# Performance work log

Hardware: AMD Instinct MI355X
Metric: run time of the kernel (lower is better)

The kernel has to match this reference:

```python
import jax, jax.numpy as jnp
import numpy as np

N_NODES = 500_000
N_EDGES = 1_000_000
EMB = 64           # config.Model.embedding_size
F = 128            # config.Model.latency_feature_size
L = 8              # config.Latency.latency_feature_length
OP_CNT = 5000
SV_CNT = 2000
ST_CNT = 16
IN_DIM = 3 * EMB + L  # 200


def setup_inputs() -> dict:
    key = jax.random.key(0)
    ks = jax.random.split(key, 24)
    s = 0.02
    inp = {
        'operation_id': jax.random.randint(ks[0], (N_NODES,), 0, OP_CNT, dtype=jnp.int32),
        'service_id':   jax.random.randint(ks[1], (N_NODES,), 0, SV_CNT, dtype=jnp.int32),
        'status_id':    jax.random.randint(ks[2], (N_NODES,), 0, ST_CNT, dtype=jnp.int32),
        'latency_feat': jax.random.normal(ks[3], (N_NODES, L), dtype=jnp.float32),
        'edge_src':     jax.random.randint(ks[4], (N_EDGES,), 0, N_NODES, dtype=jnp.int32),
        'edge_dst':     jax.random.randint(ks[5], (N_EDGES,), 0, N_NODES, dtype=jnp.int32),
        'eps':          jax.random.normal(ks[6], (N_NODES, F), dtype=jnp.float32),
        # parameters (LevelEmbedding + TreeLSTMLatencyEncoder + TreeLSTMLatencyDecoder)
        'op_embed':      jax.random.normal(ks[7],  (OP_CNT, EMB), dtype=jnp.float32) * s,
        'service_embed': jax.random.normal(ks[8],  (SV_CNT, EMB), dtype=jnp.float32) * s,
        'status_embed':  jax.random.normal(ks[9],  (ST_CNT, EMB), dtype=jnp.float32) * s,
        'enc_W1': jax.random.normal(ks[10], (IN_DIM, F), dtype=jnp.float32) * s,
        'enc_b1': jnp.zeros((F,), dtype=jnp.float32),
        'enc_W2': jax.random.normal(ks[11], (F, 2 * F), dtype=jnp.float32) * s,
        'enc_b2': jnp.zeros((2 * F,), dtype=jnp.float32),
        'dec_Wself': jax.random.normal(ks[12], (F, F), dtype=jnp.float32) * s,
        'dec_Wagg':  jax.random.normal(ks[13], (F, F), dtype=jnp.float32) * s,
        'mu_W': jax.random.normal(ks[14], (F, L), dtype=jnp.float32) * s,
        'mu_b': jnp.zeros((L,), dtype=jnp.float32),
        'lv_W': jax.random.normal(ks[15], (F, L), dtype=jnp.float32) * s,
        'lv_b': jnp.zeros((L,), dtype=jnp.float32),
        'opwise_embed': jax.random.normal(ks[16], (OP_CNT + 1, 2 * L * L), dtype=jnp.float32) * s,
    }
    return inp


def reference(operation_id, service_id, status_id, latency_feat, edge_src, edge_dst, eps,
              op_embed, service_embed, status_embed,
              enc_W1, enc_b1, enc_W2, enc_b2,
              dec_Wself, dec_Wagg, mu_W, mu_b, lv_W, lv_b, opwise_embed):
    N = latency_feat.shape[0]
    # ---- LevelEmbedding: gathers + concat ----
    feats = jnp.concatenate([
        op_embed[operation_id],
        service_embed[service_id],
        status_embed[status_id],
        latency_feat,
    ], axis=-1)  # [N, 3*EMB + L]
    # ---- TreeLSTMLatencyEncoder ----
    h = jax.nn.relu(feats @ enc_W1 + enc_b1)
    y = h @ enc_W2 + enc_b2                       # [N, 2F]
    z_mu, z_lv = jnp.split(y, 2, axis=-1)
    z_lv = jnp.tanh(z_lv)
    z = z_mu + jnp.exp(0.5 * z_lv) * eps          # reparameterize, [N, F]
    # ---- TreeLSTM decoder (one child-sum message-passing step over edges) ----
    agg = jax.ops.segment_sum(z[edge_src], edge_dst, num_segments=N)  # scatter-reduce
    yd = jax.nn.relu(z @ dec_Wself + agg @ dec_Wagg)                  # [N, F]
    mu = yd @ mu_W + mu_b   # [N, L]
    lv = yd @ lv_W + lv_b   # [N, L]
    # op-wise output transform: per-node [1,L] @ [L,L]
    w = opwise_embed[operation_id].reshape(N, L, 2 * L)
    w_mu, w_lv = w[..., :L], w[..., L:]
    mu = jnp.einsum('nl,nlk->nk', mu, w_mu)
    lv = jnp.einsum('nl,nlk->nk', lv, w_lv)
    # ---- latency_loss: gaussian NLL + opid scatter aggregation ----
    label = latency_feat
    loss = (mu - label) ** 2 / (2.0 * jnp.exp(lv) + 1e-7) + 0.5 * lv  # [N, L]
    loss_node = jnp.mean(loss, axis=1)                                 # [N]
    op_loss = jax.ops.segment_sum(loss_node, operation_id, num_segments=OP_CNT)
    op_cnt = jax.ops.segment_sum(jnp.ones((N,), jnp.int32), operation_id, num_segments=OP_CNT)
    lat_loss = jnp.mean(loss_node)
    kl = -0.5 * jnp.mean(z_lv + 1.0 - jnp.exp(z_lv) - z_mu ** 2)
    total = lat_loss + kl
    return (total, op_loss, op_cnt)
```

## Files before the change

### kernel.cpp

```cpp
#include <hip/hip_runtime.h>
#include <math.h>

#define NN 500000
#define NE 1000000
#define OPC 5000
#define NBLK_SCAN 489
#define NBLK ((NN + 127) / 128)

typedef short short8 __attribute__((ext_vector_type(8)));
typedef float f32x4 __attribute__((ext_vector_type(4)));

static __device__ __forceinline__ short f2bf(float f) {
    unsigned u = __builtin_bit_cast(unsigned, f);
    u += 0x7fffu + ((u >> 16) & 1u);
    return (short)(u >> 16);
}
static __device__ __forceinline__ float bf2f(short s) {
    unsigned u = ((unsigned)(unsigned short)s) << 16;
    return __builtin_bit_cast(float, u);
}
static __device__ __forceinline__ short8 cvt8(float4 a, float4 b) {
    short8 r;
    r[0] = f2bf(a.x); r[1] = f2bf(a.y); r[2] = f2bf(a.z); r[3] = f2bf(a.w);
    r[4] = f2bf(b.x); r[5] = f2bf(b.y); r[6] = f2bf(b.z); r[7] = f2bf(b.w);
    return r;
}
static __device__ __forceinline__ short8 ldcvt(const float* p) {
    const float4* p4 = (const float4*)p;
    return cvt8(p4[0], p4[1]);
}

__global__ void prep_kernel(const float* __restrict__ W1, const float* __restrict__ W2,
                            const float* __restrict__ Wself, const float* __restrict__ Wagg,
                            const float* __restrict__ muW, const float* __restrict__ lvW,
                            short* __restrict__ W1s, short* __restrict__ W2s,
                            short* __restrict__ Wds0, short* __restrict__ Wds1,
                            short* __restrict__ HWp)
{
    int idx = blockIdx.x * 256 + threadIdx.x;
    {
        int col = idx >> 8, r = idx & 255;
        int k = ((r >> 3) ^ (col & 7)) * 8 + (r & 7);
        W1s[idx] = (k < 200) ? f2bf(W1[k * 128 + col]) : (short)0;
    }
    {
        int col = idx >> 7, r = idx & 127;
        int k = ((r >> 3) ^ (col & 7)) * 8 + (r & 7);
        W2s[idx] = f2bf(W2[k * 256 + col]);
    }
    if (idx < 128 * 128) {
        int col = idx >> 7, r = idx & 127;
        int k = ((r >> 3) ^ (col & 7)) * 8 + (r & 7);
        Wds0[idx] = f2bf(Wself[k * 128 + col]);
        Wds1[idx] = f2bf(Wagg[k * 128 + col]);
    }
    if (idx < 16 * 128) {
        int n = idx >> 7, k = idx & 127;
        HWp[idx] = (n < 8) ? f2bf(muW[k * 8 + n]) : f2bf(lvW[k * 8 + (n - 8)]);
    }
}

__global__ __launch_bounds__(256, 2) void enc1_mfma(
    const int* __restrict__ op_id, const int* __restrict__ sv_id, const int* __restrict__ st_id,
    const float* __restrict__ lat,
    const float* __restrict__ opE, const float* __restrict__ svE, const float* __restrict__ stE,
    const short* __restrict__ W1s, const float* __restrict__ b1,
    short* __restrict__ h_bf)
{
    __shared__ __align__(16) short Bb[128 * 256];
    const int tid = threadIdx.x;
    const int lane = tid & 63, w = tid >> 6;
    const int m = lane & 15, q = lane >> 4;
    const int wbase = blockIdx.x * 128 + w * 32;

    {
        const short8* g = (const short8*)W1s;
        short8* l = (short8*)Bb;
        #pragma unroll
        for (int i = 0; i < 16; i++) l[tid + 256 * i] = g[tid + 256 * i];
    }
    __syncthreads();
    if (wbase >= NN) return;

    const int n0 = wbase + m, n1 = wbase + 16 + m;
    const size_t op0 = (size_t)op_id[n0] * 64, op1 = (size_t)op_id[n1] * 64;
    const size_t sv0 = (size_t)sv_id[n0] * 64, sv1 = (size_t)sv_id[n1] * 64;
    const size_t st0 = (size_t)st_id[n0] * 64, st1 = (size_t)st_id[n1] * 64;

    f32x4 acc[2][8];
    #pragma unroll
    for (int a2 = 0; a2 < 2; a2++)
        #pragma unroll
        for (int nf = 0; nf < 8; nf++) acc[a2][nf] = (f32x4)0.0f;

    #pragma unroll
    for (int s = 0; s < 7; s++) {
        short8 a0, a1;
        if (s < 2) {
            a0 = ldcvt(opE + op0 + s * 32 + q * 8);
            a1 = ldcvt(opE + op1 + s * 32 + q * 8);
        } else if (s < 4) {
            a0 = ldcvt(svE + sv0 + (s - 2) * 32 + q * 8);
            a1 = ldcvt(svE + sv1 + (s - 2) * 32 + q * 8);
        } else if (s < 6) {
            a0 = ldcvt(stE + st0 + (s - 4) * 32 + q * 8);
            a1 = ldcvt(stE + st1 + (s - 4) * 32 + q * 8);
        } else {
            if (q == 0) {
                a0 = ldcvt(lat + (size_t)n0 * 8);
                a1 = ldcvt(lat + (size_t)n1 * 8);
            } else {
                #pragma unroll
                for (int i = 0; i < 8; i++) { a0[i] = 0; a1[i] = 0; }
            }
        }
        const int slot = ((4 * s + q) ^ (m & 7)) * 8;
        #pragma unroll
        for (int nf = 0; nf < 8; nf++) {
            const short8 b = *(const short8*)&Bb[(nf * 16 + m) * 256 + slot];
            acc[0][nf] = __builtin_amdgcn_mfma_f32_16x16x32_bf16(a0, b, acc[0][nf], 0, 0, 0);
            acc[1][nf] = __builtin_amdgcn_mfma_f32_16x16x32_bf16(a1, b, acc[1][nf], 0, 0, 0);
        }
    }
    #pragma unroll
    for (int a2 = 0; a2 < 2; a2++)
        #pragma unroll
        for (int nf = 0; nf < 8; nf++) {
            int col = nf * 16 + m;
            float bb = b1[col];
            #pragma unroll
            for (int r = 0; r < 4; r++) {
                int node = wbase + a2 * 16 + q * 4 + r;
                h_bf[(size_t)node * 128 + col] = f2bf(fmaxf(acc[a2][nf][r] + bb, 0.0f));
            }
        }
}

__global__ __launch_bounds__(256, 2) void enc2_mfma(
    const short* __restrict__ h_bf, const short* __restrict__ W2s, const float* __restrict__ b2,
    const float* __restrict__ eps, short* __restrict__ z_bf, float* __restrict__ kl_sum)
{
    __shared__ __align__(16) short Bb[256 * 128];
    const int tid = threadIdx.x;
    const int lane = tid & 63, w = tid >> 6;
    const int m = lane & 15, q = lane >> 4;
    const int wbase = blockIdx.x * 128 + w * 32;

    {
        const short8* g = (const short8*)W2s;
        short8* l = (short8*)Bb;
        #pragma unroll
        for (int i = 0; i < 16; i++) l[tid + 256 * i] = g[tid + 256 * i];
    }
    __syncthreads();
    if (wbase >= NN) return;

    short8 a[2][4];
    #pragma unroll
    for (int s = 0; s < 4; s++) {
        a[0][s] = *(const short8*)(h_bf + (size_t)(wbase + m) * 128 + s * 32 + q * 8);
        a[1][s] = *(const short8*)(h_bf + (size_t)(wbase + 16 + m) * 128 + s * 32 + q * 8);
    }

    f32x4 acc[2][16];
    #pragma unroll
    for (int a2 = 0; a2 < 2; a2++)
        #pragma unroll
        for (int nf = 0; nf < 16; nf++) acc[a2][nf] = (f32x4)0.0f;

    #pragma unroll
    for (int s = 0; s < 4; s++) {
        const int slot = ((4 * s + q) ^ (m & 7)) * 8;
        #pragma unroll
        for (int nf = 0; nf < 16; nf++) {
            const short8 b = *(const short8*)&Bb[(nf * 16 + m) * 128 + slot];
            acc[0][nf] = __builtin_amdgcn_mfma_f32_16x16x32_bf16(a[0][s], b, acc[0][nf], 0, 0, 0);
            acc[1][nf] = __builtin_amdgcn_mfma_f32_16x16x32_bf16(a[1][s], b, acc[1][nf], 0, 0, 0);
        }
    }

    float kll = 0.0f;
    #pragma unroll
    for (int a2 = 0; a2 < 2; a2++)
        #pragma unroll
        for (int nf = 0; nf < 8; nf++) {
            int col = nf * 16 + m;
            float bm = b2[col], bl = b2[col + 128];
            #pragma unroll
            for (int r = 0; r < 4; r++) {
                int node = wbase + a2 * 16 + q * 4 + r;
                float mu = acc[a2][nf][r] + bm;
                float lv = tanhf(acc[a2][nf + 8][r] + bl);
                float e  = eps[(size_t)node * 128 + col];
                z_bf[(size_t)node * 128 + col] = f2bf(mu + expf(0.5f * lv) * e);
                kll += lv + 1.0f - expf(lv) - mu * mu;
            }
        }
    #pragma unroll
    for (int off = 32; off > 0; off >>= 1) kll += __shfl_down(kll, off);
    if (lane == 0) atomicAdd(kl_sum, kll);
}

__global__ void hist_kernel(const int* __restrict__ edst, int* __restrict__ cnt)
{
    int e = blockIdx.x * 256 + threadIdx.x;
    if (e < NE) atomicAdd(&cnt[edst[e]], 1);
}

__global__ void scan1_kernel(const int* __restrict__ cnt, int* __restrict__ bsum)
{
    __shared__ int ls[256];
    int b = blockIdx.x, tid = threadIdx.x;
    int idx0 = b * 1024 + tid * 4;
    int s = 0;
    #pragma unroll
    for (int i = 0; i < 4; i++) { int idx = idx0 + i; if (idx < NN) s += cnt[idx]; }
    ls[tid] = s; __syncthreads();
    for (int off = 128; off > 0; off >>= 1) {
        if (tid < off) ls[tid] += ls[tid + off];
        __syncthreads();
    }
    if (tid == 0) bsum[b] = ls[0];
}

__global__ void scan2_kernel(int* __restrict__ bsum, int* __restrict__ rowstart)
{
    __shared__ int ls[512];
    int tid = threadIdx.x;
    int v = (tid < NBLK_SCAN) ? bsum[tid] : 0;
    ls[tid] = v; __syncthreads();
    for (int off = 1; off < 512; off <<= 1) {
        int t = 0;
        if (tid >= off) t = ls[tid - off];
        __syncthreads();
        ls[tid] += t;
        __syncthreads();
    }
    if (tid < NBLK_SCAN) bsum[tid] = (tid == 0) ? 0 : ls[tid - 1];
    if (tid == 0) rowstart[NN] = NE;
}

__global__ void scan3_kernel(const int* __restrict__ cnt, const int* __restrict__ bsum,
                             int* __restrict__ rowstart, int* __restrict__ cursor)
{
    __shared__ int ls[256];
    int b = blockIdx.x, tid = threadIdx.x;
    int idx0 = b * 1024 + tid * 4;
    int v[4]; int s = 0;
    #pragma unroll
    for (int i = 0; i < 4; i++) { int idx = idx0 + i; v[i] = (idx < NN) ? cnt[idx] : 0; s += v[i]; }
    ls[tid] = s; __syncthreads();
    for (int off = 1; off < 256; off <<= 1) {
        int t = 0;
        if (tid >= off) t = ls[tid - off];
        __syncthreads();
        ls[tid] += t;
        __syncthreads();
    }
    int ex = ls[tid] - s + bsum[b];
    #pragma unroll
    for (int i = 0; i < 4; i++) {
        int idx = idx0 + i;
        if (idx < NN) { rowstart[idx] = ex; cursor[idx] = ex; }
        ex += v[i];
    }
}

__global__ void fill_kernel(const int* __restrict__ esrc, const int* __restrict__ edst,
                            int* __restrict__ cursor, int* __restrict__ csr)
{
    int e = blockIdx.x * 256 + threadIdx.x;
    if (e < NE) {
        int pos = atomicAdd(&cursor[edst[e]], 1);
        csr[pos] = esrc[e];
    }
}

__global__ __launch_bounds__(256, 2) void dec_mfma(
    const short* __restrict__ z_bf, const int* __restrict__ rowstart, const int* __restrict__ csr,
    const short* __restrict__ Wds0, const short* __restrict__ Wds1, const short* __restrict__ HWp,
    const float* __restrict__ mub, const float* __restrict__ lvb,
    const float* __restrict__ opwise, const int* __restrict__ op_id,
    const float* __restrict__ lat,
    float* __restrict__ op_loss, float* __restrict__ op_cnt,
    float* __restrict__ loss_sum)
{
    __shared__ __align__(16) short regionA[128 * 128];
    __shared__ __align__(16) char  regionB[32768];
    short* Bb  = (short*)regionB;
    short* hw  = (short*)regionB;
    float* mlv = (float*)(regionB + 4608);

    const int tid = threadIdx.x;
    const int lane = tid & 63, w = tid >> 6;
    const int m = lane & 15, q = lane >> 4;
    const int bbase = blockIdx.x * 128;
    const int wbase = bbase + w * 32;
    const bool wv = (wbase < NN);

    {
        const short8* g = (const short8*)Wds0;
        short8* l = (short8*)Bb;
        #pragma unroll
        for (int i = 0; i < 8; i++) l[tid + 256 * i] = g[tid + 256 * i];
    }
    {
        int nodeL = tid & 127, hh = tid >> 7;
        int n = bbase + nodeL;
        float a[64];
        #pragma unroll
        for (int i = 0; i < 64; i++) a[i] = 0.0f;
        if (n < NN) {
            int r0 = rowstart[n], r1 = rowstart[n + 1];
            for (int e = r0; e < r1; e++) {
                const short8* zp = (const short8*)(z_bf + (size_t)csr[e] * 128 + hh * 64);
                #pragma unroll
                for (int j = 0; j < 8; j++) {
                    short8 v = zp[j];
                    #pragma unroll
                    for (int i = 0; i < 8; i++) a[j * 8 + i] += bf2f(v[i]);
                }
            }
        }
        #pragma unroll
        for (int j = 0; j < 8; j++) {
            int slot = ((hh * 8 + j) ^ (nodeL & 7)) * 8;
            short8 o;
            #pragma unroll
            for (int i = 0; i < 8; i++) o[i] = f2bf(a[j * 8 + i]);
            *(short8*)&regionA[nodeL * 128 + slot] = o;
        }
    }
    __syncthreads();

    f32x4 acc[2][8];
    #pragma unroll
    for (int a2 = 0; a2 < 2; a2++)
        #pragma unroll
        for (int nf = 0; nf < 8; nf++) acc[a2][nf] = (f32x4)0.0f;

    if (wv) {
        short8 az[2][4];
        #pragma unroll
        for (int s = 0; s < 4; s++) {
            az[0][s] = *(const short8*)(z_bf + (size_t)(wbase + m) * 128 + s * 32 + q * 8);
            az[1][s] = *(const short8*)(z_bf + (size_t)(wbase + 16 + m) * 128 + s * 32 + q * 8);
        }
        #pragma unroll
        for (int s = 0; s < 4; s++) {
            const int slot = ((4 * s + q) ^ (m & 7)) * 8;
            #pragma unroll
            for (int nf = 0; nf < 8; nf++) {
                const short8 b = *(const short8*)&Bb[(nf * 16 + m) * 128 + slot];
                acc[0][nf] = __builtin_amdgcn_mfma_f32_16x16x32_bf16(az[0][s], b, acc[0][nf], 0, 0, 0);
                acc[1][nf] = __builtin_amdgcn_mfma_f32_16x16x32_bf16(az[1][s], b, acc[1][nf], 0, 0, 0);
            }
        }
    }
    __syncthreads();

    {
        const short8* g = (const short8*)Wds1;
        short8* l = (short8*)Bb;
        #pragma unroll
        for (int i = 0; i < 8; i++) l[tid + 256 * i] = g[tid + 256 * i];
    }
    __syncthreads();

    if (wv) {
        #pragma unroll
        for (int s = 0; s < 4; s++) {
            const int slot = ((4 * s + q) ^ (m & 7)) * 8;
            const short8 a0 = *(const short8*)&regionA[(w * 32 + m) * 128 + slot];
            const short8 a1 = *(const short8*)&regionA[(w * 32 + 16 + m) * 128 + slot];
            #pragma unroll
            for (int nf = 0; nf < 8; nf++) {
                const short8 b = *(const short8*)&Bb[(nf * 16 + m) * 128 + slot];
                acc[0][nf] = __builtin_amdgcn_mfma_f32_16x16x32_bf16(a0, b, acc[0][nf], 0, 0, 0);
                acc[1][nf] = __builtin_amdgcn_mfma_f32_16x16x32_bf16(a1, b, acc[1][nf], 0, 0, 0);
            }
        }
    }
    __syncthreads();

    if (wv) {
        #pragma unroll
        for (int a2 = 0; a2 < 2; a2++)
            #pragma unroll
            for (int nf = 0; nf < 8; nf++) {
                int c = nf * 2 + (m >> 3);
                #pragma unroll
                for (int r = 0; r < 4; r++) {
                    int node = w * 32 + a2 * 16 + q * 4 + r;
                    regionA[node * 128 + ((c ^ (node & 7)) * 8) + (m & 7)] =
                        f2bf(fmaxf(acc[a2][nf][r], 0.0f));
                }
            }
    }
    {
        int nn = tid >> 4, c = tid & 15;
        *(short8*)&hw[nn * 136 + c * 8] = *(const short8*)(HWp + nn * 128 + c * 8);
    }
    __syncthreads();

    if (wv) {
        f32x4 h0 = (f32x4)0.0f, h1 = (f32x4)0.0f;
        #pragma unroll
        for (int s2 = 0; s2 < 4; s2++) {
            const int slot = ((4 * s2 + q) ^ (m & 7)) * 8;
            short8 a0 = *(const short8*)&regionA[(w * 32 + m) * 128 + slot];
            short8 a1 = *(const short8*)&regionA[(w * 32 + 16 + m) * 128 + slot];
            short8 b  = *(const short8*)&hw[m * 136 + s2 * 32 + q * 8];
            h0 = __builtin_amdgcn_mfma_f32_16x16x32_bf16(a0, b, h0, 0, 0, 0);
            h1 = __builtin_amdgcn_mfma_f32_16x16x32_bf16(a1, b, h1, 0, 0, 0);
        }
        float hb = (m < 8) ? mub[m] : lvb[m - 8];
        #pragma unroll
        for (int r = 0; r < 4; r++) {
            mlv[(w * 32 + q * 4 + r) * 16 + m]      = h0[r] + hb;
            mlv[(w * 32 + 16 + q * 4 + r) * 16 + m] = h1[r] + hb;
        }
    }
    __syncthreads();

    float lsum = 0.0f;
    if (tid < 128 && bbase + tid < NN) {
        const int t = tid;
        const int n = bbase + t;
        const int op = op_id[n];
        const float4* w4 = (const float4*)(opwise + (size_t)op * 128);
        float mout[8], lout[8];
        #pragma unroll
        for (int k = 0; k < 8; k++) { mout[k] = 0.0f; lout[k] = 0.0f; }
        #pragma unroll
        for (int l = 0; l < 8; l++) {
            float mv = mlv[t * 16 + l];
            float vv = mlv[t * 16 + 8 + l];
            float4 a = w4[l * 4 + 0];
            float4 b = w4[l * 4 + 1];
            float4 c = w4[l * 4 + 2];
            float4 d = w4[l * 4 + 3];
            mout[0] = fmaf(mv, a.x, mout[0]); mout[1] = fmaf(mv, a.y, mout[1]);
            mout[2] = fmaf(mv, a.z, mout[2]); mout[3] = fmaf(mv, a.w, mout[3]);
            mout[4] = fmaf(mv, b.x, mout[4]); mout[5] = fmaf(mv, b.y, mout[5]);
            mout[6] = fmaf(mv, b.z, mout[6]); mout[7] = fmaf(mv, b.w, mout[7]);
            lout[0] = fmaf(vv, c.x, lout[0]); lout[1] = fmaf(vv, c.y, lout[1]);
            lout[2] = fmaf(vv, c.z, lout[2]); lout[3] = fmaf(vv, c.w, lout[3]);
            lout[4] = fmaf(vv, d.x, lout[4]); lout[5] = fmaf(vv, d.y, lout[5]);
            lout[6] = fmaf(vv, d.z, lout[6]); lout[7] = fmaf(vv, d.w, lout[7]);
        }
        const float4* lp = (const float4*)(lat + (size_t)n * 8);
        float4 lb0 = lp[0], lb1 = lp[1];
        float labels[8] = {lb0.x, lb0.y, lb0.z, lb0.w, lb1.x, lb1.y, lb1.z, lb1.w};
        float lnode = 0.0f;
        #pragma unroll
        for (int k = 0; k < 8; k++) {
            float diff = mout[k] - labels[k];
            lnode += diff * diff / (2.0f * expf(lout[k]) + 1e-7f) + 0.5f * lout[k];
        }
        lnode *= 0.125f;
        atomicAdd(&op_loss[op], lnode);
        atomicAdd(&op_cnt[op], 1.0f);
        lsum = lnode;
    }
    #pragma unroll
    for (int off = 32; off > 0; off >>= 1) lsum += __shfl_down(lsum, off);
    if (lane == 0) atomicAdd(loss_sum, lsum);
}

__global__ void final_kernel(const float* __restrict__ accum, float* __restrict__ out)
{
    out[0] = accum[1] / (float)NN - 0.5f * (accum[0] / (float)((size_t)NN * 128));
}

extern "C" void kernel_launch(void* const* d_in, const int* in_sizes, int n_in,
                              void* d_out, int out_size, void* d_ws, size_t ws_size,
                              hipStream_t stream) {
    const int*   op_id  = (const int*)  d_in[0];
    const int*   sv_id  = (const int*)  d_in[1];
    const int*   st_id  = (const int*)  d_in[2];
    const float* lat    = (const float*)d_in[3];
    const int*   esrc   = (const int*)  d_in[4];
    const int*   edst   = (const int*)  d_in[5];
    const float* eps    = (const float*)d_in[6];
    const float* opE    = (const float*)d_in[7];
    const float* svE    = (const float*)d_in[8];
    const float* stE    = (const float*)d_in[9];
    const float* W1     = (const float*)d_in[10];
    const float* b1     = (const float*)d_in[11];
    const float* W2     = (const float*)d_in[12];
    const float* b2     = (const float*)d_in[13];
    const float* Wself  = (const float*)d_in[14];
    const float* Wagg   = (const float*)d_in[15];
    const float* muW    = (const float*)d_in[16];
    const float* mub    = (const float*)d_in[17];
    const float* lvW    = (const float*)d_in[18];
    const float* lvb    = (const float*)d_in[19];
    const float* opwise = (const float*)d_in[20];

    char* wsb = (char*)d_ws;
    short* W1s      = (short*)(wsb + 0);
    short* W2s      = (short*)(wsb + 65536);
    short* Wds0     = (short*)(wsb + 131072);
    short* Wds1     = (short*)(wsb + 163840);
    short* HWp      = (short*)(wsb + 196608);
    float* accum    = (float*)(wsb + 204800);
    int*   cnt      = (int*)  (wsb + (4  << 20));
    int*   rowstart = (int*)  (wsb + (6  << 20));
    int*   cursor   = (int*)  (wsb + (9  << 20));
    int*   csr      = (int*)  (wsb + (12 << 20));
    int*   bsum     = (int*)  (wsb + (16 << 20));
    short* h_bf     = (short*)(wsb + (32  << 20));
    short* z_bf     = (short*)(wsb + (160ull << 20));
    float* out      = (float*)d_out;

    hipMemsetAsync(d_out, 0, (size_t)out_size * sizeof(float), stream);
    hipMemsetAsync(accum, 0, 2 * sizeof(float), stream);
    hipMemsetAsync(cnt, 0, (size_t)NN * sizeof(int), stream);

    prep_kernel<<<128, 256, 0, stream>>>(W1, W2, Wself, Wagg, muW, lvW,
                                         W1s, W2s, Wds0, Wds1, HWp);

    hist_kernel<<<(NE + 255) / 256, 256, 0, stream>>>(edst, cnt);
    scan1_kernel<<<NBLK_SCAN, 256, 0, stream>>>(cnt, bsum);
    scan2_kernel<<<1, 512, 0, stream>>>(bsum, rowstart);
    scan3_kernel<<<NBLK_SCAN, 256, 0, stream>>>(cnt, bsum, rowstart, cursor);
    fill_kernel<<<(NE + 255) / 256, 256, 0, stream>>>(esrc, edst, cursor, csr);

    enc1_mfma<<<NBLK, 256, 0, stream>>>(op_id, sv_id, st_id, lat, opE, svE, stE, W1s, b1, h_bf);
    enc2_mfma<<<NBLK, 256, 0, stream>>>(h_bf, W2s, b2, eps, z_bf, accum + 0);
    dec_mfma<<<NBLK, 256, 0, stream>>>(z_bf, rowstart, csr, Wds0, Wds1, HWp, mub, lvb,
                                       opwise, op_id, lat,
                                       out + 1, out + 1 + OPC, accum + 1);
    final_kernel<<<1, 1, 0, stream>>>(accum, out);
}
```

Measured before the change: 1.152 ms.

## Stage encoder outputs through LDS for coalesced h and z stores

Both encoder kernels now write their MFMA accumulator tiles into shared memory and then emit fully coalesced 16-byte row stores of h and z, instead of scattered 2-byte stores in MFMA layout. In enc2, the eps read is also made coalesced by packing mu and exp(0.5*lv) as bf16 pairs in LDS and doing the reparameterization in the store phase. tanh is replaced by an exp/rcp formulation with fast intrinsics. This adds extra block barriers, rounds mu and the scale to bf16 before the FMA, and keeps waves that are out of range alive so they can reach the barriers.

```diff
diff --git a/kernel.cpp b/kernel.cpp
--- a/kernel.cpp
+++ b/kernel.cpp
@@ -71,7 +71,9 @@
     const int tid = threadIdx.x;
     const int lane = tid & 63, w = tid >> 6;
     const int m = lane & 15, q = lane >> 4;
-    const int wbase = blockIdx.x * 128 + w * 32;
+    const int bbase = blockIdx.x * 128;
+    const int wbase = bbase + w * 32;
+    const bool wv = (wbase < NN);
 
     {
         const short8* g = (const short8*)W1s;
@@ -80,12 +82,6 @@
         for (int i = 0; i < 16; i++) l[tid + 256 * i] = g[tid + 256 * i];
     }
     __syncthreads();
-    if (wbase >= NN) return;
-
-    const int n0 = wbase + m, n1 = wbase + 16 + m;
-    const size_t op0 = (size_t)op_id[n0] * 64, op1 = (size_t)op_id[n1] * 64;
-    const size_t sv0 = (size_t)sv_id[n0] * 64, sv1 = (size_t)sv_id[n1] * 64;
-    const size_t st0 = (size_t)st_id[n0] * 64, st1 = (size_t)st_id[n1] * 64;
 
     f32x4 acc[2][8];
     #pragma unroll
@@ -93,47 +89,70 @@
         #pragma unroll
         for (int nf = 0; nf < 8; nf++) acc[a2][nf] = (f32x4)0.0f;
 
-    #pragma unroll
-    for (int s = 0; s < 7; s++) {
-        short8 a0, a1;
-        if (s < 2) {
-            a0 = ldcvt(opE + op0 + s * 32 + q * 8);
-            a1 = ldcvt(opE + op1 + s * 32 + q * 8);
-        } else if (s < 4) {
-            a0 = ldcvt(svE + sv0 + (s - 2) * 32 + q * 8);
-            a1 = ldcvt(svE + sv1 + (s - 2) * 32 + q * 8);
-        } else if (s < 6) {
-            a0 = ldcvt(stE + st0 + (s - 4) * 32 + q * 8);
-            a1 = ldcvt(stE + st1 + (s - 4) * 32 + q * 8);
-        } else {
-            if (q == 0) {
-                a0 = ldcvt(lat + (size_t)n0 * 8);
-                a1 = ldcvt(lat + (size_t)n1 * 8);
+    if (wv) {
+        const int n0 = wbase + m, n1 = wbase + 16 + m;
+        const size_t op0 = (size_t)op_id[n0] * 64, op1 = (size_t)op_id[n1] * 64;
+        const size_t sv0 = (size_t)sv_id[n0] * 64, sv1 = (size_t)sv_id[n1] * 64;
+        const size_t st0 = (size_t)st_id[n0] * 64, st1 = (size_t)st_id[n1] * 64;
+
+        #pragma unroll
+        for (int s = 0; s < 7; s++) {
+            short8 a0, a1;
+            if (s < 2) {
+                a0 = ldcvt(opE + op0 + s * 32 + q * 8);
+                a1 = ldcvt(opE + op1 + s * 32 + q * 8);
+            } else if (s < 4) {
+                a0 = ldcvt(svE + sv0 + (s - 2) * 32 + q * 8);
+                a1 = ldcvt(svE + sv1 + (s - 2) * 32 + q * 8);
+            } else if (s < 6) {
+                a0 = ldcvt(stE + st0 + (s - 4) * 32 + q * 8);
+                a1 = ldcvt(stE + st1 + (s - 4) * 32 + q * 8);
             } else {
-                #pragma unroll
-                for (int i = 0; i < 8; i++) { a0[i] = 0; a1[i] = 0; }
-            }
-        }
-        const int slot = ((4 * s + q) ^ (m & 7)) * 8;
-        #pragma unroll
-        for (int nf = 0; nf < 8; nf++) {
-            const short8 b = *(const short8*)&Bb[(nf * 16 + m) * 256 + slot];
-            acc[0][nf] = __builtin_amdgcn_mfma_f32_16x16x32_bf16(a0, b, acc[0][nf], 0, 0, 0);
-            acc[1][nf] = __builtin_amdgcn_mfma_f32_16x16x32_bf16(a1, b, acc[1][nf], 0, 0, 0);
-        }
-    }
-    #pragma unroll
-    for (int a2 = 0; a2 < 2; a2++)
+                if (q == 0) {
+                    a0 = ldcvt(lat + (size_t)n0 * 8);
+                    a1 = ldcvt(lat + (size_t)n1 * 8);
+                } else {
+                    #pragma unroll
+                    for (int i = 0; i < 8; i++) { a0[i] = 0; a1[i] = 0; }
+                }
+            }
+            const int slot = ((4 * s + q) ^ (m & 7)) * 8;
+            #pragma unroll
+            for (int nf = 0; nf < 8; nf++) {
+                const short8 b = *(const short8*)&Bb[(nf * 16 + m) * 256 + slot];
+                acc[0][nf] = __builtin_amdgcn_mfma_f32_16x16x32_bf16(a0, b, acc[0][nf], 0, 0, 0);
+                acc[1][nf] = __builtin_amdgcn_mfma_f32_16x16x32_bf16(a1, b, acc[1][nf], 0, 0, 0);
+            }
+        }
+    }
+    __syncthreads();
+
+    if (wv) {
         #pragma unroll
         for (int nf = 0; nf < 8; nf++) {
             int col = nf * 16 + m;
             float bb = b1[col];
             #pragma unroll
-            for (int r = 0; r < 4; r++) {
-                int node = wbase + a2 * 16 + q * 4 + r;
-                h_bf[(size_t)node * 128 + col] = f2bf(fmaxf(acc[a2][nf][r] + bb, 0.0f));
-            }
-        }
+            for (int a2 = 0; a2 < 2; a2++)
+                #pragma unroll
+                for (int r = 0; r < 4; r++) {
+                    int g = w * 32 + a2 * 16 + q * 4 + r;
+                    Bb[g * 136 + col] = f2bf(fmaxf(acc[a2][nf][r] + bb, 0.0f));
+                }
+        }
+    }
+    __syncthreads();
+
+    {
+        int g = tid >> 1, cb = (tid & 1) * 64;
+        int node = bbase + g;
+        if (node < NN) {
+            short8* dst = (short8*)(h_bf + (size_t)node * 128 + cb);
+            const short8* src = (const short8*)&Bb[g * 136 + cb];
+            #pragma unroll
+            for (int i = 0; i < 8; i++) dst[i] = src[i];
+        }
+    }
 }
 
 __global__ __launch_bounds__(256, 2) void enc2_mfma(
@@ -141,26 +160,21 @@
     const float* __restrict__ eps, short* __restrict__ z_bf, float* __restrict__ kl_sum)
 {
     __shared__ __align__(16) short Bb[256 * 128];
+    int* ldsI = (int*)Bb;
     const int tid = threadIdx.x;
     const int lane = tid & 63, w = tid >> 6;
     const int m = lane & 15, q = lane >> 4;
-    const int wbase = blockIdx.x * 128 + w * 32;
-
-    {
-        const short8* g = (const short8*)W2s;
+    const int bbase = blockIdx.x * 128;
+    const int wbase = bbase + w * 32;
+    const bool wv = (wbase < NN);
+
+    {
+        const short8* g8 = (const short8*)W2s;
         short8* l = (short8*)Bb;
         #pragma unroll
-        for (int i = 0; i < 16; i++) l[tid + 256 * i] = g[tid + 256 * i];
-    }
-    __syncthreads();
-    if (wbase >= NN) return;
-
-    short8 a[2][4];
-    #pragma unroll
-    for (int s = 0; s < 4; s++) {
-        a[0][s] = *(const short8*)(h_bf + (size_t)(wbase + m) * 128 + s * 32 + q * 8);
-        a[1][s] = *(const short8*)(h_bf + (size_t)(wbase + 16 + m) * 128 + s * 32 + q * 8);
-    }
+        for (int i = 0; i < 16; i++) l[tid + 256 * i] = g8[tid + 256 * i];
+    }
+    __syncthreads();
 
     f32x4 acc[2][16];
     #pragma unroll
@@ -168,34 +182,74 @@
         #pragma unroll
         for (int nf = 0; nf < 16; nf++) acc[a2][nf] = (f32x4)0.0f;
 
-    #pragma unroll
-    for (int s = 0; s < 4; s++) {
-        const int slot = ((4 * s + q) ^ (m & 7)) * 8;
-        #pragma unroll
-        for (int nf = 0; nf < 16; nf++) {
-            const short8 b = *(const short8*)&Bb[(nf * 16 + m) * 128 + slot];
-            acc[0][nf] = __builtin_amdgcn_mfma_f32_16x16x32_bf16(a[0][s], b, acc[0][nf], 0, 0, 0);
-            acc[1][nf] = __builtin_amdgcn_mfma_f32_16x16x32_bf16(a[1][s], b, acc[1][nf], 0, 0, 0);
-        }
-    }
+    if (wv) {
+        short8 a[2][4];
+        #pragma unroll
+        for (int s = 0; s < 4; s++) {
+            a[0][s] = *(const short8*)(h_bf + (size_t)(wbase + m) * 128 + s * 32 + q * 8);
+            a[1][s] = *(const short8*)(h_bf + (size_t)(wbase + 16 + m) * 128 + s * 32 + q * 8);
+        }
+        #pragma unroll
+        for (int s = 0; s < 4; s++) {
+            const int slot = ((4 * s + q) ^ (m & 7)) * 8;
+            #pragma unroll
+            for (int nf = 0; nf < 16; nf++) {
+                const short8 b = *(const short8*)&Bb[(nf * 16 + m) * 128 + slot];
+                acc[0][nf] = __builtin_amdgcn_mfma_f32_16x16x32_bf16(a[0][s], b, acc[0][nf], 0, 0, 0);
+                acc[1][nf] = __builtin_amdgcn_mfma_f32_16x16x32_bf16(a[1][s], b, acc[1][nf], 0, 0, 0);
+            }
+        }
+    }
+    __syncthreads();
 
     float kll = 0.0f;
     #pragma unroll
-    for (int a2 = 0; a2 < 2; a2++)
-        #pragma unroll
-        for (int nf = 0; nf < 8; nf++) {
-            int col = nf * 16 + m;
-            float bm = b2[col], bl = b2[col + 128];
-            #pragma unroll
-            for (int r = 0; r < 4; r++) {
-                int node = wbase + a2 * 16 + q * 4 + r;
-                float mu = acc[a2][nf][r] + bm;
-                float lv = tanhf(acc[a2][nf + 8][r] + bl);
-                float e  = eps[(size_t)node * 128 + col];
-                z_bf[(size_t)node * 128 + col] = f2bf(mu + expf(0.5f * lv) * e);
-                kll += lv + 1.0f - expf(lv) - mu * mu;
-            }
-        }
+    for (int a2 = 0; a2 < 2; a2++) {
+        if (wv) {
+            #pragma unroll
+            for (int nf = 0; nf < 8; nf++) {
+                int col = nf * 16 + m;
+                float bm = b2[col], bl = b2[col + 128];
+                #pragma unroll
+                for (int r = 0; r < 4; r++) {
+                    float mu = acc[a2][nf][r] + bm;
+                    float lr = acc[a2][nf + 8][r] + bl;
+                    float e2 = __expf(2.0f * lr);
+                    float t  = 1.0f - 2.0f * __builtin_amdgcn_rcpf(e2 + 1.0f);
+                    float s  = __expf(0.5f * t);
+                    kll += t + 1.0f - s * s - mu * mu;
+                    int pk = (int)(unsigned short)f2bf(mu)
+                           | ((int)(unsigned short)f2bf(s) << 16);
+                    ldsI[(w * 16 + q * 4 + r) * 132 + col] = pk;
+                }
+            }
+        }
+        __syncthreads();
+        {
+            int g = tid >> 2, cb = (tid & 3) * 32;
+            int node = bbase + (g >> 4) * 32 + a2 * 16 + (g & 15);
+            if (node < NN) {
+                const float4* ep = (const float4*)(eps + (size_t)node * 128 + cb);
+                const int4*   lp = (const int4*)&ldsI[g * 132 + cb];
+                #pragma unroll
+                for (int c = 0; c < 4; c++) {
+                    int4 va = lp[c * 2], vb = lp[c * 2 + 1];
+                    float4 ea = ep[c * 2], eb = ep[c * 2 + 1];
+                    short8 o;
+                    o[0] = f2bf(fmaf(bf2f((short)(va.x >> 16)), ea.x, bf2f((short)va.x)));
+                    o[1] = f2bf(fmaf(bf2f((short)(va.y >> 16)), ea.y, bf2f((short)va.y)));
+                    o[2] = f2bf(fmaf(bf2f((short)(va.z >> 16)), ea.z, bf2f((short)va.z)));
+                    o[3] = f2bf(fmaf(bf2f((short)(va.w >> 16)), ea.w, bf2f((short)va.w)));
+                    o[4] = f2bf(fmaf(bf2f((short)(vb.x >> 16)), eb.x, bf2f((short)vb.x)));
+                    o[5] = f2bf(fmaf(bf2f((short)(vb.y >> 16)), eb.y, bf2f((short)vb.y)));
+                    o[6] = f2bf(fmaf(bf2f((short)(vb.z >> 16)), eb.z, bf2f((short)vb.z)));
+                    o[7] = f2bf(fmaf(bf2f((short)(vb.w >> 16)), eb.w, bf2f((short)vb.w)));
+                    *(short8*)(z_bf + (size_t)node * 128 + cb + c * 8) = o;
+                }
+            }
+        }
+        __syncthreads();
+    }
     #pragma unroll
     for (int off = 32; off > 0; off >>= 1) kll += __shfl_down(kll, off);
     if (lane == 0) atomicAdd(kl_sum, kll);
```

Measured after the change: 1.047 ms. -9.2%, faster.
